# Optimization experiments

Measured on AMD Instinct MI355X. Metric: run time of the kernel, lower is better.

## Reference

```python
import jax, jax.numpy as jnp
import numpy as np


def setup_inputs() -> dict:
    key = jax.random.key(0)
    ks = jax.random.split(key, 13)
    B, CTX, H, ENC, BALL, T = 65536, 128, 64, 64, 2, 64
    IN = 2 + BALL + ENC  # 68
    s = lambda *sh: 1.0 / np.sqrt(sh[-1])
    return {
        "context": jax.random.normal(ks[0], (B, CTX), jnp.float32),
        "target_encoding": jax.random.normal(ks[1], (B, ENC), jnp.float32),
        "ball_land_xy": jax.random.normal(ks[2], (B, BALL), jnp.float32),
        "Wh_ctx": jax.random.normal(ks[3], (H, CTX), jnp.float32) * s(CTX),
        "bh_ctx": jax.random.normal(ks[4], (H,), jnp.float32) * 0.01,
        "Wc_ctx": jax.random.normal(ks[5], (H, CTX), jnp.float32) * s(CTX),
        "bc_ctx": jax.random.normal(ks[6], (H,), jnp.float32) * 0.01,
        "W_ih": jax.random.normal(ks[7], (4 * H, IN), jnp.float32) * s(IN),
        "W_hh": jax.random.normal(ks[8], (4 * H, H), jnp.float32) * s(H),
        "b_ih": jax.random.normal(ks[9], (4 * H,), jnp.float32) * 0.01,
        "b_hh": jax.random.normal(ks[10], (4 * H,), jnp.float32) * 0.01,
        "W_out": jax.random.normal(ks[11], (2, H), jnp.float32) * s(H),
        "b_out": jax.random.normal(ks[12], (2,), jnp.float32) * 0.01,
        "max_frames": T,
    }


def reference(context, target_encoding, ball_land_xy,
              Wh_ctx, bh_ctx, Wc_ctx, bc_ctx,
              W_ih, W_hh, b_ih, b_hh, W_out, b_out, max_frames):
    H = W_hh.shape[1]
    # initial hidden / cell state from fused context (num_layers=1, so squeeze the layer dim)
    h0 = context @ Wh_ctx.T + bh_ctx  # (B, H)
    c0 = context @ Wc_ctx.T + bc_ctx  # (B, H)
    B = context.shape[0]

    # decoder input per step = [prev_disp(2), ball_land_xy(2), target_encoding(64)];
    # ball/encoding part is constant across steps -> precompute its gate contribution
    W_prev = W_ih[:, :2]            # (4H, 2) columns acting on prev_disp
    W_stat = W_ih[:, 2:]            # (4H, 2+ENC)
    static = jnp.concatenate([ball_land_xy, target_encoding], axis=-1)
    gates_static = static @ W_stat.T + b_ih + b_hh  # (B, 4H)

    prev0 = jnp.zeros((B, 2), context.dtype)

    def step(carry, _):
        h, c, prev = carry
        gates = prev @ W_prev.T + h @ W_hh.T + gates_static  # (B, 4H)
        i, f, g, o = jnp.split(gates, 4, axis=-1)            # torch gate order i,f,g,o
        i = jax.nn.sigmoid(i)
        f = jax.nn.sigmoid(f)
        g = jnp.tanh(g)
        o = jax.nn.sigmoid(o)
        c = f * c + i * g
        h = o * jnp.tanh(c)
        pred = h @ W_out.T + b_out                           # (B, 2)
        # prev_disp = pred.detach() in the original
        return (h, c, jax.lax.stop_gradient(pred)), pred

    _, preds = jax.lax.scan(step, (h0, c0, prev0), None, length=max_frames)
    return jnp.transpose(preds, (1, 0, 2))  # (B, max_frames, 2)
```

## Files before the change

kernel.cpp:

```cpp
#include <hip/hip_runtime.h>
#include <hip/hip_bf16.h>
#include <stdint.h>


typedef unsigned short u16;
typedef unsigned int u32;
typedef __bf16 bf16x8 __attribute__((ext_vector_type(8)));
typedef u16 u16x8 __attribute__((ext_vector_type(8)));
typedef float f32x4 __attribute__((ext_vector_type(4)));
typedef float f32x2 __attribute__((ext_vector_type(2)));

#define MFMA16(a, b, c) __builtin_amdgcn_mfma_f32_16x16x32_bf16((a), (b), (c), 0, 0, 0)

#define SCL_SIG (-1.442695040888963f)
#define SCL_TANH (2.885390081777927f)

__device__ __forceinline__ u16 f2bf(float f) {
  __bf16 h = (__bf16)f;
  return __builtin_bit_cast(u16, h);
}
__device__ __forceinline__ float bf2f(u16 u) {
  return __builtin_bit_cast(float, ((u32)u) << 16);
}
__device__ __forceinline__ u32 pkbf(float lo, float hi) {
  union { __bf16 b[2]; u32 u; } p;
  p.b[0] = (__bf16)lo;
  p.b[1] = (__bf16)hi;
  return p.u;
}
__device__ __forceinline__ bf16x8 ldfrag_g(const u16* p) {
  u16x8 v = *(const u16x8*)p;
  return __builtin_bit_cast(bf16x8, v);
}
__device__ __forceinline__ void split8(const float* v, bf16x8& hi, bf16x8& lo) {
  union { u16 s[8]; bf16x8 b; } H, L;
#pragma unroll
  for (int i = 0; i < 8; i++) {
    u16 h = f2bf(v[i]);
    H.s[i] = h;
    L.s[i] = f2bf(v[i] - bf2f(h));
  }
  hi = H.b;
  lo = L.b;
}

__device__ __forceinline__ void nonlin4(const f32x4 ai, const f32x4 af, const f32x4 ag,
                                        const f32x4 ao, f32x4& crow, u32& w0h, u32& w1h,
                                        u32& w0l, u32& w1l) {
  float hi[4], lo[4];
#pragma unroll
  for (int q = 0; q < 4; q++) {
    float iv = __builtin_amdgcn_rcpf(1.f + __builtin_amdgcn_exp2f(ai[q]));
    float fv = __builtin_amdgcn_rcpf(1.f + __builtin_amdgcn_exp2f(af[q]));
    float ov = __builtin_amdgcn_rcpf(1.f + __builtin_amdgcn_exp2f(ao[q]));
    float rg = __builtin_amdgcn_rcpf(1.f + __builtin_amdgcn_exp2f(ag[q]));
    float gv = __builtin_fmaf(rg, -2.f, 1.f);
    float cc = __builtin_fmaf(fv, crow[q], iv * gv);
    crow[q] = cc;
    float r2 = __builtin_amdgcn_rcpf(1.f + __builtin_amdgcn_exp2f(cc * SCL_TANH));
    float hh = __builtin_fmaf(r2, ov * -2.f, ov);
    u16 h16 = f2bf(hh);
    hi[q] = bf2f(h16);
    lo[q] = hh - hi[q];
  }
  w0h = pkbf(hi[0], hi[1]);
  w1h = pkbf(hi[2], hi[3]);
  w0l = pkbf(lo[0], lo[1]);
  w1l = pkbf(lo[2], lo[3]);
}

__global__ void setup_k(const float* __restrict__ Wh_ctx, const float* __restrict__ Wc_ctx,
                        const float* __restrict__ W_ih, const float* __restrict__ W_hh,
                        const float* __restrict__ b_ih, const float* __restrict__ b_hh,
                        const float* __restrict__ W_out, const float* __restrict__ b_out,
                        u16* __restrict__ weffH, u16* __restrict__ weffL,
                        u16* __restrict__ whhH, u16* __restrict__ whhL,
                        u16* __restrict__ wstatH, u16* __restrict__ wstatL,
                        u16* __restrict__ whcH, u16* __restrict__ whcL,
                        u16* __restrict__ wccH, u16* __restrict__ wccL,
                        float* __restrict__ bsum, float* __restrict__ wpbv) {
  int gr = (int)threadIdx.x;
  const int gate = gr >> 6;
  const float s = (gate == 2) ? SCL_TANH : SCL_SIG;
  float wp0 = W_ih[gr * 68 + 0];
  float wp1 = W_ih[gr * 68 + 1];
  for (int k = 0; k < 64; k++) {
    float whh = s * W_hh[gr * 64 + k];
    u16 h = f2bf(whh);
    whhH[gr * 64 + k] = h;
    whhL[gr * 64 + k] = f2bf(whh - bf2f(h));
    float we = s * (W_hh[gr * 64 + k] + wp0 * W_out[k] + wp1 * W_out[64 + k]);
    u16 eh = f2bf(we);
    weffH[gr * 64 + k] = eh;
    weffL[gr * 64 + k] = f2bf(we - bf2f(eh));
  }
  for (int k = 0; k < 96; k++) {
    float v = (k < 66) ? s * W_ih[gr * 68 + 2 + k] : 0.f;
    u16 h = f2bf(v);
    wstatH[gr * 96 + k] = h;
    wstatL[gr * 96 + k] = f2bf(v - bf2f(h));
  }
  float wpb_ = s * (wp0 * b_out[0] + wp1 * b_out[1]);
  wpbv[gr] = wpb_;
  bsum[gr] = s * (b_ih[gr] + b_hh[gr]) + wpb_;
  if (gr < 64) {
    for (int k = 0; k < 128; k++) {
      float a = Wh_ctx[gr * 128 + k];
      u16 ah = f2bf(a);
      whcH[gr * 128 + k] = ah;
      whcL[gr * 128 + k] = f2bf(a - bf2f(ah));
      float b = Wc_ctx[gr * 128 + k];
      u16 bh_ = f2bf(b);
      wccH[gr * 128 + k] = bh_;
      wccL[gr * 128 + k] = f2bf(b - bf2f(bh_));
    }
  }
}

#define HFRAG(base, f) \
  ldfrag_g((const u16*)((const char*)(base) + c * 128 + (((16 * g) + 64 * (f)) ^ sw4)))

#define HWRITE(base, grp, w0, w1)                                \
  do {                                                           \
    char* bp_ = (char*)(base) + c * 128;                         \
    *(u32*)(bp_ + ((32 * (grp) + 8 * g) ^ sw4)) = (w0);          \
    *(u32*)(bp_ + ((32 * (grp) + 8 * g + 4) ^ sw4)) = (w1);      \
  } while (0)

__global__ __launch_bounds__(256, 3) void traj_main(
    const float* __restrict__ ctx, const float* __restrict__ enc,
    const float* __restrict__ ball, const float* __restrict__ bh,
    const float* __restrict__ bc, const float* __restrict__ bout,
    const float* __restrict__ woutf, const u16* __restrict__ weffH,
    const u16* __restrict__ weffL, const u16* __restrict__ whhH,
    const u16* __restrict__ whhL, const u16* __restrict__ wstatH,
    const u16* __restrict__ wstatL, const u16* __restrict__ whcH,
    const u16* __restrict__ whcL, const u16* __restrict__ wccH,
    const u16* __restrict__ wccL, const float* __restrict__ bsum,
    const float* __restrict__ wpbv, float* __restrict__ out) {
  __shared__ __align__(16) u16 hH_sh[2][16 * 64];
  __shared__ __align__(16) u16 hL_sh[2][16 * 64];
  __shared__ __align__(16) float p_sh[16 * 64 * 2];

  const int tid = (int)threadIdx.x;
  const int lane = tid & 63;
  const int w = tid >> 6;
  const int c = lane & 15;
  const int g = lane >> 4;
  const int sw4 = (c & 7) << 4;
  const int b0 = (int)blockIdx.x * 16;
  const size_t row = (size_t)(b0 + c);

  bf16x8 xcH[4], xcL[4];
#pragma unroll
  for (int kk = 0; kk < 4; kk++) {
    const float* p = ctx + row * 128 + 32 * kk + 8 * g;
    f32x4 a = *(const f32x4*)p;
    f32x4 b = *(const f32x4*)(p + 4);
    float v[8] = {a[0], a[1], a[2], a[3], b[0], b[1], b[2], b[3]};
    split8(v, xcH[kk], xcL[kk]);
  }

  {
    f32x4 acc = *(const f32x4*)(bh + 16 * w + 4 * g);
#pragma unroll
    for (int kk = 0; kk < 4; kk++) {
      bf16x8 aH = ldfrag_g(whcH + (16 * w + c) * 128 + 32 * kk + 8 * g);
      bf16x8 aL = ldfrag_g(whcL + (16 * w + c) * 128 + 32 * kk + 8 * g);
      acc = MFMA16(aH, xcH[kk], acc);
      acc = MFMA16(aH, xcL[kk], acc);
      acc = MFMA16(aL, xcH[kk], acc);
    }
    float hi_[4], lo_[4];
#pragma unroll
    for (int q = 0; q < 4; q++) {
      u16 h16 = f2bf(acc[q]);
      hi_[q] = bf2f(h16);
      lo_[q] = acc[q] - hi_[q];
    }
    HWRITE(hH_sh[0], w, pkbf(hi_[0], hi_[1]), pkbf(hi_[2], hi_[3]));
    HWRITE(hL_sh[0], w, pkbf(lo_[0], lo_[1]), pkbf(lo_[2], lo_[3]));
  }

  f32x4 cst;
  {
    f32x4 acc = *(const f32x4*)(bc + 16 * w + 4 * g);
#pragma unroll
    for (int kk = 0; kk < 4; kk++) {
      bf16x8 aH = ldfrag_g(wccH + (16 * w + c) * 128 + 32 * kk + 8 * g);
      bf16x8 aL = ldfrag_g(wccL + (16 * w + c) * 128 + 32 * kk + 8 * g);
      acc = MFMA16(aH, xcH[kk], acc);
      acc = MFMA16(aH, xcL[kk], acc);
      acc = MFMA16(aL, xcH[kk], acc);
    }
    cst = acc;
  }

  bf16x8 xsH[3], xsL[3];
#pragma unroll
  for (int kk = 0; kk < 3; kk++) {
    float v[8];
#pragma unroll
    for (int j = 0; j < 8; j++) {
      int k = 32 * kk + 8 * g + j;
      float val = 0.f;
      if (k < 2) val = ball[row * 2 + k];
      else if (k < 66) val = enc[row * 64 + (k - 2)];
      v[j] = val;
    }
    split8(v, xsH[kk], xsL[kk]);
  }

  f32x4 gsf[4];
#pragma unroll
  for (int j = 0; j < 4; j++) {
    const int tl = 4 * j + w;
    f32x4 acc = *(const f32x4*)(bsum + 16 * tl + 4 * g);
#pragma unroll
    for (int kk = 0; kk < 3; kk++) {
      bf16x8 aH = ldfrag_g(wstatH + (16 * tl + c) * 96 + 32 * kk + 8 * g);
      bf16x8 aL = ldfrag_g(wstatL + (16 * tl + c) * 96 + 32 * kk + 8 * g);
      acc = MFMA16(aH, xsH[kk], acc);
      acc = MFMA16(aH, xsL[kk], acc);
      acc = MFMA16(aL, xsH[kk], acc);
    }
    gsf[j] = acc;
  }

  bf16x8 wof[2];
#pragma unroll
  for (int f = 0; f < 2; f++) {
    float v[8];
#pragma unroll
    for (int j = 0; j < 8; j++) {
      int k = 32 * f + 8 * g + j;
      v[j] = (c < 2) ? woutf[c * 64 + k] : 0.f;
    }
    bf16x8 dummy;
    split8(v, wof[f], dummy);
  }
  const float bo0 = bout[0], bo1 = bout[1];

  bf16x8 wfH[4][2], wfL[4][2];
#pragma unroll
  for (int j = 0; j < 4; j++) {
    const int tl = 4 * j + w;
#pragma unroll
    for (int f = 0; f < 2; f++) {
      wfH[j][f] = ldfrag_g(weffH + (16 * tl + c) * 64 + 32 * f + 8 * g);
      wfL[j][f] = ldfrag_g(weffL + (16 * tl + c) * 64 + 32 * f + 8 * g);
    }
  }

  __syncthreads();

  {
    bf16x8 hh0 = HFRAG(hH_sh[0], 0), hh1 = HFRAG(hH_sh[0], 1);
    bf16x8 hl0 = HFRAG(hL_sh[0], 0), hl1 = HFRAG(hL_sh[0], 1);
    f32x4 av[4];
#pragma unroll
    for (int j = 0; j < 4; j++) {
      const int tl = 4 * j + w;
      f32x4 acc = gsf[j] - *(const f32x4*)(wpbv + 16 * tl + 4 * g);
      bf16x8 aH0 = ldfrag_g(whhH + (16 * tl + c) * 64 + 8 * g);
      bf16x8 aH1 = ldfrag_g(whhH + (16 * tl + c) * 64 + 32 + 8 * g);
      bf16x8 aL0 = ldfrag_g(whhL + (16 * tl + c) * 64 + 8 * g);
      bf16x8 aL1 = ldfrag_g(whhL + (16 * tl + c) * 64 + 32 + 8 * g);
      acc = MFMA16(aH0, hh0, acc);
      acc = MFMA16(aH1, hh1, acc);
      acc = MFMA16(aH0, hl0, acc);
      acc = MFMA16(aH1, hl1, acc);
      acc = MFMA16(aL0, hh0, acc);
      acc = MFMA16(aL1, hh1, acc);
      av[j] = acc;
    }
    u32 w0h, w1h, w0l, w1l;
    nonlin4(av[0], av[1], av[2], av[3], cst, w0h, w1h, w0l, w1l);
    HWRITE(hH_sh[1], w, w0h, w1h);
    HWRITE(hL_sh[1], w, w0l, w1l);
    __syncthreads();
  }

#pragma unroll 1
  for (int k = 1; k < 64; k++) {
    const int rb = k & 1, wb = rb ^ 1;
    bf16x8 hh0 = HFRAG(hH_sh[rb], 0), hh1 = HFRAG(hH_sh[rb], 1);
    bf16x8 hl0 = HFRAG(hL_sh[rb], 0), hl1 = HFRAG(hL_sh[rb], 1);
    if (((k - 1) & 3) == w) {
      f32x4 pacc = {bo0, bo1, 0.f, 0.f};
      pacc = MFMA16(wof[0], hh0, pacc);
      pacc = MFMA16(wof[1], hh1, pacc);
      if (g == 0) {
        f32x2 pr = {pacc[0], pacc[1]};
        *(f32x2*)((char*)p_sh + c * 512 + (((k - 1) * 8) ^ ((c & 7) << 3))) = pr;
      }
    }
    f32x4 av[4];
#pragma unroll
    for (int j = 0; j < 4; j++) {
      f32x4 acc = gsf[j];
      acc = MFMA16(wfH[j][0], hh0, acc);
      acc = MFMA16(wfH[j][1], hh1, acc);
      acc = MFMA16(wfH[j][0], hl0, acc);
      acc = MFMA16(wfH[j][1], hl1, acc);
      acc = MFMA16(wfL[j][0], hh0, acc);
      acc = MFMA16(wfL[j][1], hh1, acc);
      av[j] = acc;
    }
    u32 w0h, w1h, w0l, w1l;
    nonlin4(av[0], av[1], av[2], av[3], cst, w0h, w1h, w0l, w1l);
    HWRITE(hH_sh[wb], w, w0h, w1h);
    HWRITE(hL_sh[wb], w, w0l, w1l);
    __syncthreads();
  }

  if (w == 3) {
    bf16x8 hh0 = HFRAG(hH_sh[0], 0), hh1 = HFRAG(hH_sh[0], 1);
    f32x4 pacc = {bo0, bo1, 0.f, 0.f};
    pacc = MFMA16(wof[0], hh0, pacc);
    pacc = MFMA16(wof[1], hh1, pacc);
    if (g == 0) {
      f32x2 pr = {pacc[0], pacc[1]};
      *(f32x2*)((char*)p_sh + c * 512 + ((63 * 8) ^ ((c & 7) << 3))) = pr;
    }
  }
  __syncthreads();

#pragma unroll
  for (int p = 0; p < 4; p++) {
    const int r = 4 * p + w;
    f32x2 v = *(const f32x2*)((const char*)p_sh + r * 512 + ((lane * 8) ^ ((r & 7) << 3)));
    *(f32x2*)(out + (size_t)(b0 + r) * 128 + lane * 2) = v;
  }
}

extern "C" void kernel_launch(void* const* d_in, const int* in_sizes, int n_in,
                              void* d_out, int out_size, void* d_ws, size_t ws_size,
                              hipStream_t stream) {
  const float* ctx = (const float*)d_in[0];
  const float* enc = (const float*)d_in[1];
  const float* ball = (const float*)d_in[2];
  const float* Wh = (const float*)d_in[3];
  const float* bh = (const float*)d_in[4];
  const float* Wc = (const float*)d_in[5];
  const float* bc = (const float*)d_in[6];
  const float* Wih = (const float*)d_in[7];
  const float* Whh = (const float*)d_in[8];
  const float* bih = (const float*)d_in[9];
  const float* bhh = (const float*)d_in[10];
  const float* Wout = (const float*)d_in[11];
  const float* bout = (const float*)d_in[12];
  float* out = (float*)d_out;

  char* ws = (char*)d_ws;
  u16* weffH = (u16*)(ws + 0);
  u16* weffL = (u16*)(ws + 32768);
  u16* whhH = (u16*)(ws + 65536);
  u16* whhL = (u16*)(ws + 98304);
  u16* wstatH = (u16*)(ws + 131072);
  u16* wstatL = (u16*)(ws + 180224);
  u16* whcH = (u16*)(ws + 229376);
  u16* whcL = (u16*)(ws + 245760);
  u16* wccH = (u16*)(ws + 262144);
  u16* wccL = (u16*)(ws + 278528);
  float* bsum = (float*)(ws + 294912);
  float* wpbv = (float*)(ws + 295936);

  const int B = in_sizes[0] / 128;

  setup_k<<<1, 256, 0, stream>>>(Wh, Wc, Wih, Whh, bih, bhh, Wout, bout, weffH, weffL,
                                 whhH, whhL, wstatH, wstatL, whcH, whcL, wccH, wccL,
                                 bsum, wpbv);
  traj_main<<<B / 16, 256, 0, stream>>>(ctx, enc, ball, bh, bc, bout, Wout, weffH, weffL,
                                        whhH, whhL, wstatH, wstatL, whcH, whcL, wccH,
                                        wccL, bsum, wpbv, out);
}
```

Before: 633.9 us.

## Process two independent 16-row batch tiles per block to interleave recurrent chains

Each block now handles 32 batch rows as two independent 16-row tiles (A and B) that share the register-resident weight fragments and barriers. Interleaving two independent MFMA dependency chains per step is meant to hide MFMA and nonlinearity latency, and it halves the number of barriers per unit of work. In exchange register pressure roughly doubles, so launch bounds drop from 3 to 2 blocks per CU and the grid halves, which lowers occupancy.

```diff
diff --git a/kernel.cpp b/kernel.cpp
--- a/kernel.cpp
+++ b/kernel.cpp
@@ -127,7 +127,7 @@
     *(u32*)(bp_ + ((32 * (grp) + 8 * g + 4) ^ sw4)) = (w1);      \
   } while (0)
 
-__global__ __launch_bounds__(256, 3) void traj_main(
+__global__ __launch_bounds__(256, 2) void traj_main(
     const float* __restrict__ ctx, const float* __restrict__ enc,
     const float* __restrict__ ball, const float* __restrict__ bh,
     const float* __restrict__ bc, const float* __restrict__ bout,
@@ -138,9 +138,9 @@
     const u16* __restrict__ whcL, const u16* __restrict__ wccH,
     const u16* __restrict__ wccL, const float* __restrict__ bsum,
     const float* __restrict__ wpbv, float* __restrict__ out) {
-  __shared__ __align__(16) u16 hH_sh[2][16 * 64];
-  __shared__ __align__(16) u16 hL_sh[2][16 * 64];
-  __shared__ __align__(16) float p_sh[16 * 64 * 2];
+  __shared__ __align__(16) u16 hH_sh[2][2][16 * 64];
+  __shared__ __align__(16) u16 hL_sh[2][2][16 * 64];
+  __shared__ __align__(16) float p_sh[2][16 * 64 * 2];
 
   const int tid = (int)threadIdx.x;
   const int lane = tid & 63;
@@ -148,83 +148,119 @@
   const int c = lane & 15;
   const int g = lane >> 4;
   const int sw4 = (c & 7) << 4;
-  const int b0 = (int)blockIdx.x * 16;
-  const size_t row = (size_t)(b0 + c);
-
-  bf16x8 xcH[4], xcL[4];
+  const int b0 = (int)blockIdx.x * 32;
+  const size_t rowA = (size_t)(b0 + c);
+  const size_t rowB = (size_t)(b0 + 16 + c);
+
+  bf16x8 xcHA[4], xcLA[4], xcHB[4], xcLB[4];
 #pragma unroll
   for (int kk = 0; kk < 4; kk++) {
-    const float* p = ctx + row * 128 + 32 * kk + 8 * g;
-    f32x4 a = *(const f32x4*)p;
-    f32x4 b = *(const f32x4*)(p + 4);
-    float v[8] = {a[0], a[1], a[2], a[3], b[0], b[1], b[2], b[3]};
-    split8(v, xcH[kk], xcL[kk]);
+    {
+      const float* p = ctx + rowA * 128 + 32 * kk + 8 * g;
+      f32x4 a = *(const f32x4*)p;
+      f32x4 b = *(const f32x4*)(p + 4);
+      float v[8] = {a[0], a[1], a[2], a[3], b[0], b[1], b[2], b[3]};
+      split8(v, xcHA[kk], xcLA[kk]);
+    }
+    {
+      const float* p = ctx + rowB * 128 + 32 * kk + 8 * g;
+      f32x4 a = *(const f32x4*)p;
+      f32x4 b = *(const f32x4*)(p + 4);
+      float v[8] = {a[0], a[1], a[2], a[3], b[0], b[1], b[2], b[3]};
+      split8(v, xcHB[kk], xcLB[kk]);
+    }
   }
 
   {
-    f32x4 acc = *(const f32x4*)(bh + 16 * w + 4 * g);
+    f32x4 accA = *(const f32x4*)(bh + 16 * w + 4 * g);
+    f32x4 accB = accA;
 #pragma unroll
     for (int kk = 0; kk < 4; kk++) {
       bf16x8 aH = ldfrag_g(whcH + (16 * w + c) * 128 + 32 * kk + 8 * g);
       bf16x8 aL = ldfrag_g(whcL + (16 * w + c) * 128 + 32 * kk + 8 * g);
-      acc = MFMA16(aH, xcH[kk], acc);
-      acc = MFMA16(aH, xcL[kk], acc);
-      acc = MFMA16(aL, xcH[kk], acc);
-    }
-    float hi_[4], lo_[4];
+      accA = MFMA16(aH, xcHA[kk], accA);
+      accA = MFMA16(aH, xcLA[kk], accA);
+      accA = MFMA16(aL, xcHA[kk], accA);
+      accB = MFMA16(aH, xcHB[kk], accB);
+      accB = MFMA16(aH, xcLB[kk], accB);
+      accB = MFMA16(aL, xcHB[kk], accB);
+    }
+    float hiA[4], loA[4], hiB[4], loB[4];
 #pragma unroll
     for (int q = 0; q < 4; q++) {
-      u16 h16 = f2bf(acc[q]);
-      hi_[q] = bf2f(h16);
-      lo_[q] = acc[q] - hi_[q];
-    }
-    HWRITE(hH_sh[0], w, pkbf(hi_[0], hi_[1]), pkbf(hi_[2], hi_[3]));
-    HWRITE(hL_sh[0], w, pkbf(lo_[0], lo_[1]), pkbf(lo_[2], lo_[3]));
-  }
-
-  f32x4 cst;
+      u16 hA = f2bf(accA[q]);
+      hiA[q] = bf2f(hA);
+      loA[q] = accA[q] - hiA[q];
+      u16 hB = f2bf(accB[q]);
+      hiB[q] = bf2f(hB);
+      loB[q] = accB[q] - hiB[q];
+    }
+    HWRITE(hH_sh[0][0], w, pkbf(hiA[0], hiA[1]), pkbf(hiA[2], hiA[3]));
+    HWRITE(hL_sh[0][0], w, pkbf(loA[0], loA[1]), pkbf(loA[2], loA[3]));
+    HWRITE(hH_sh[1][0], w, pkbf(hiB[0], hiB[1]), pkbf(hiB[2], hiB[3]));
+    HWRITE(hL_sh[1][0], w, pkbf(loB[0], loB[1]), pkbf(loB[2], loB[3]));
+  }
+
+  f32x4 cstA, cstB;
   {
-    f32x4 acc = *(const f32x4*)(bc + 16 * w + 4 * g);
+    f32x4 accA = *(const f32x4*)(bc + 16 * w + 4 * g);
+    f32x4 accB = accA;
 #pragma unroll
     for (int kk = 0; kk < 4; kk++) {
       bf16x8 aH = ldfrag_g(wccH + (16 * w + c) * 128 + 32 * kk + 8 * g);
       bf16x8 aL = ldfrag_g(wccL + (16 * w + c) * 128 + 32 * kk + 8 * g);
-      acc = MFMA16(aH, xcH[kk], acc);
-      acc = MFMA16(aH, xcL[kk], acc);
-      acc = MFMA16(aL, xcH[kk], acc);
-    }
-    cst = acc;
-  }
-
-  bf16x8 xsH[3], xsL[3];
+      accA = MFMA16(aH, xcHA[kk], accA);
+      accA = MFMA16(aH, xcLA[kk], accA);
+      accA = MFMA16(aL, xcHA[kk], accA);
+      accB = MFMA16(aH, xcHB[kk], accB);
+      accB = MFMA16(aH, xcLB[kk], accB);
+      accB = MFMA16(aL, xcHB[kk], accB);
+    }
+    cstA = accA;
+    cstB = accB;
+  }
+
+  bf16x8 xsHA[3], xsLA[3], xsHB[3], xsLB[3];
 #pragma unroll
   for (int kk = 0; kk < 3; kk++) {
-    float v[8];
+    float vA[8], vB[8];
 #pragma unroll
     for (int j = 0; j < 8; j++) {
       int k = 32 * kk + 8 * g + j;
-      float val = 0.f;
-      if (k < 2) val = ball[row * 2 + k];
-      else if (k < 66) val = enc[row * 64 + (k - 2)];
-      v[j] = val;
-    }
-    split8(v, xsH[kk], xsL[kk]);
-  }
-
-  f32x4 gsf[4];
+      float a = 0.f, b = 0.f;
+      if (k < 2) {
+        a = ball[rowA * 2 + k];
+        b = ball[rowB * 2 + k];
+      } else if (k < 66) {
+        a = enc[rowA * 64 + (k - 2)];
+        b = enc[rowB * 64 + (k - 2)];
+      }
+      vA[j] = a;
+      vB[j] = b;
+    }
+    split8(vA, xsHA[kk], xsLA[kk]);
+    split8(vB, xsHB[kk], xsLB[kk]);
+  }
+
+  f32x4 gsfA[4], gsfB[4];
 #pragma unroll
   for (int j = 0; j < 4; j++) {
     const int tl = 4 * j + w;
-    f32x4 acc = *(const f32x4*)(bsum + 16 * tl + 4 * g);
+    f32x4 accA = *(const f32x4*)(bsum + 16 * tl + 4 * g);
+    f32x4 accB = accA;
 #pragma unroll
     for (int kk = 0; kk < 3; kk++) {
       bf16x8 aH = ldfrag_g(wstatH + (16 * tl + c) * 96 + 32 * kk + 8 * g);
       bf16x8 aL = ldfrag_g(wstatL + (16 * tl + c) * 96 + 32 * kk + 8 * g);
-      acc = MFMA16(aH, xsH[kk], acc);
-      acc = MFMA16(aH, xsL[kk], acc);
-      acc = MFMA16(aL, xsH[kk], acc);
-    }
-    gsf[j] = acc;
+      accA = MFMA16(aH, xsHA[kk], accA);
+      accA = MFMA16(aH, xsLA[kk], accA);
+      accA = MFMA16(aL, xsHA[kk], accA);
+      accB = MFMA16(aH, xsHB[kk], accB);
+      accB = MFMA16(aH, xsLB[kk], accB);
+      accB = MFMA16(aL, xsHB[kk], accB);
+    }
+    gsfA[j] = accA;
+    gsfB[j] = accB;
   }
 
   bf16x8 wof[2];
@@ -255,82 +291,127 @@
   __syncthreads();
 
   {
-    bf16x8 hh0 = HFRAG(hH_sh[0], 0), hh1 = HFRAG(hH_sh[0], 1);
-    bf16x8 hl0 = HFRAG(hL_sh[0], 0), hl1 = HFRAG(hL_sh[0], 1);
-    f32x4 av[4];
+    bf16x8 hhA0 = HFRAG(hH_sh[0][0], 0), hhA1 = HFRAG(hH_sh[0][0], 1);
+    bf16x8 hlA0 = HFRAG(hL_sh[0][0], 0), hlA1 = HFRAG(hL_sh[0][0], 1);
+    bf16x8 hhB0 = HFRAG(hH_sh[1][0], 0), hhB1 = HFRAG(hH_sh[1][0], 1);
+    bf16x8 hlB0 = HFRAG(hL_sh[1][0], 0), hlB1 = HFRAG(hL_sh[1][0], 1);
+    f32x4 avA[4], avB[4];
 #pragma unroll
     for (int j = 0; j < 4; j++) {
       const int tl = 4 * j + w;
-      f32x4 acc = gsf[j] - *(const f32x4*)(wpbv + 16 * tl + 4 * g);
+      f32x4 base = *(const f32x4*)(wpbv + 16 * tl + 4 * g);
+      f32x4 accA = gsfA[j] - base;
+      f32x4 accB = gsfB[j] - base;
       bf16x8 aH0 = ldfrag_g(whhH + (16 * tl + c) * 64 + 8 * g);
       bf16x8 aH1 = ldfrag_g(whhH + (16 * tl + c) * 64 + 32 + 8 * g);
       bf16x8 aL0 = ldfrag_g(whhL + (16 * tl + c) * 64 + 8 * g);
       bf16x8 aL1 = ldfrag_g(whhL + (16 * tl + c) * 64 + 32 + 8 * g);
-      acc = MFMA16(aH0, hh0, acc);
-      acc = MFMA16(aH1, hh1, acc);
-      acc = MFMA16(aH0, hl0, acc);
-      acc = MFMA16(aH1, hl1, acc);
-      acc = MFMA16(aL0, hh0, acc);
-      acc = MFMA16(aL1, hh1, acc);
-      av[j] = acc;
+      accA = MFMA16(aH0, hhA0, accA);
+      accA = MFMA16(aH1, hhA1, accA);
+      accA = MFMA16(aH0, hlA0, accA);
+      accA = MFMA16(aH1, hlA1, accA);
+      accA = MFMA16(aL0, hhA0, accA);
+      accA = MFMA16(aL1, hhA1, accA);
+      accB = MFMA16(aH0, hhB0, accB);
+      accB = MFMA16(aH1, hhB1, accB);
+      accB = MFMA16(aH0, hlB0, accB);
+      accB = MFMA16(aH1, hlB1, accB);
+      accB = MFMA16(aL0, hhB0, accB);
+      accB = MFMA16(aL1, hhB1, accB);
+      avA[j] = accA;
+      avB[j] = accB;
     }
     u32 w0h, w1h, w0l, w1l;
-    nonlin4(av[0], av[1], av[2], av[3], cst, w0h, w1h, w0l, w1l);
-    HWRITE(hH_sh[1], w, w0h, w1h);
-    HWRITE(hL_sh[1], w, w0l, w1l);
+    nonlin4(avA[0], avA[1], avA[2], avA[3], cstA, w0h, w1h, w0l, w1l);
+    HWRITE(hH_sh[0][1], w, w0h, w1h);
+    HWRITE(hL_sh[0][1], w, w0l, w1l);
+    nonlin4(avB[0], avB[1], avB[2], avB[3], cstB, w0h, w1h, w0l, w1l);
+    HWRITE(hH_sh[1][1], w, w0h, w1h);
+    HWRITE(hL_sh[1][1], w, w0l, w1l);
     __syncthreads();
   }
 
 #pragma unroll 1
   for (int k = 1; k < 64; k++) {
     const int rb = k & 1, wb = rb ^ 1;
-    bf16x8 hh0 = HFRAG(hH_sh[rb], 0), hh1 = HFRAG(hH_sh[rb], 1);
-    bf16x8 hl0 = HFRAG(hL_sh[rb], 0), hl1 = HFRAG(hL_sh[rb], 1);
+    bf16x8 hhA0 = HFRAG(hH_sh[0][rb], 0), hhA1 = HFRAG(hH_sh[0][rb], 1);
+    bf16x8 hlA0 = HFRAG(hL_sh[0][rb], 0), hlA1 = HFRAG(hL_sh[0][rb], 1);
+    bf16x8 hhB0 = HFRAG(hH_sh[1][rb], 0), hhB1 = HFRAG(hH_sh[1][rb], 1);
+    bf16x8 hlB0 = HFRAG(hL_sh[1][rb], 0), hlB1 = HFRAG(hL_sh[1][rb], 1);
     if (((k - 1) & 3) == w) {
-      f32x4 pacc = {bo0, bo1, 0.f, 0.f};
-      pacc = MFMA16(wof[0], hh0, pacc);
-      pacc = MFMA16(wof[1], hh1, pacc);
+      f32x4 pA = {bo0, bo1, 0.f, 0.f};
+      pA = MFMA16(wof[0], hhA0, pA);
+      pA = MFMA16(wof[1], hhA1, pA);
+      f32x4 pB = {bo0, bo1, 0.f, 0.f};
+      pB = MFMA16(wof[0], hhB0, pB);
+      pB = MFMA16(wof[1], hhB1, pB);
       if (g == 0) {
-        f32x2 pr = {pacc[0], pacc[1]};
-        *(f32x2*)((char*)p_sh + c * 512 + (((k - 1) * 8) ^ ((c & 7) << 3))) = pr;
+        f32x2 prA = {pA[0], pA[1]};
+        *(f32x2*)((char*)&p_sh[0][0] + c * 512 + (((k - 1) * 8) ^ ((c & 7) << 3))) = prA;
+        f32x2 prB = {pB[0], pB[1]};
+        *(f32x2*)((char*)&p_sh[1][0] + c * 512 + (((k - 1) * 8) ^ ((c & 7) << 3))) = prB;
       }
     }
-    f32x4 av[4];
+    f32x4 avA[4], avB[4];
 #pragma unroll
     for (int j = 0; j < 4; j++) {
-      f32x4 acc = gsf[j];
-      acc = MFMA16(wfH[j][0], hh0, acc);
-      acc = MFMA16(wfH[j][1], hh1, acc);
-      acc = MFMA16(wfH[j][0], hl0, acc);
-      acc = MFMA16(wfH[j][1], hl1, acc);
-      acc = MFMA16(wfL[j][0], hh0, acc);
-      acc = MFMA16(wfL[j][1], hh1, acc);
-      av[j] = acc;
+      f32x4 acc = gsfA[j];
+      acc = MFMA16(wfH[j][0], hhA0, acc);
+      acc = MFMA16(wfH[j][1], hhA1, acc);
+      acc = MFMA16(wfH[j][0], hlA0, acc);
+      acc = MFMA16(wfH[j][1], hlA1, acc);
+      acc = MFMA16(wfL[j][0], hhA0, acc);
+      acc = MFMA16(wfL[j][1], hhA1, acc);
+      avA[j] = acc;
+    }
+#pragma unroll
+    for (int j = 0; j < 4; j++) {
+      f32x4 acc = gsfB[j];
+      acc = MFMA16(wfH[j][0], hhB0, acc);
+      acc = MFMA16(wfH[j][1], hhB1, acc);
+      acc = MFMA16(wfH[j][0], hlB0, acc);
+      acc = MFMA16(wfH[j][1], hlB1, acc);
+      acc = MFMA16(wfL[j][0], hhB0, acc);
+      acc = MFMA16(wfL[j][1], hhB1, acc);
+      avB[j] = acc;
     }
     u32 w0h, w1h, w0l, w1l;
-    nonlin4(av[0], av[1], av[2], av[3], cst, w0h, w1h, w0l, w1l);
-    HWRITE(hH_sh[wb], w, w0h, w1h);
-    HWRITE(hL_sh[wb], w, w0l, w1l);
+    nonlin4(avA[0], avA[1], avA[2], avA[3], cstA, w0h, w1h, w0l, w1l);
+    HWRITE(hH_sh[0][wb], w, w0h, w1h);
+    HWRITE(hL_sh[0][wb], w, w0l, w1l);
+    nonlin4(avB[0], avB[1], avB[2], avB[3], cstB, w0h, w1h, w0l, w1l);
+    HWRITE(hH_sh[1][wb], w, w0h, w1h);
+    HWRITE(hL_sh[1][wb], w, w0l, w1l);
     __syncthreads();
   }
 
   if (w == 3) {
-    bf16x8 hh0 = HFRAG(hH_sh[0], 0), hh1 = HFRAG(hH_sh[0], 1);
-    f32x4 pacc = {bo0, bo1, 0.f, 0.f};
-    pacc = MFMA16(wof[0], hh0, pacc);
-    pacc = MFMA16(wof[1], hh1, pacc);
+    bf16x8 hhA0 = HFRAG(hH_sh[0][0], 0), hhA1 = HFRAG(hH_sh[0][0], 1);
+    bf16x8 hhB0 = HFRAG(hH_sh[1][0], 0), hhB1 = HFRAG(hH_sh[1][0], 1);
+    f32x4 pA = {bo0, bo1, 0.f, 0.f};
+    pA = MFMA16(wof[0], hhA0, pA);
+    pA = MFMA16(wof[1], hhA1, pA);
+    f32x4 pB = {bo0, bo1, 0.f, 0.f};
+    pB = MFMA16(wof[0], hhB0, pB);
+    pB = MFMA16(wof[1], hhB1, pB);
     if (g == 0) {
-      f32x2 pr = {pacc[0], pacc[1]};
-      *(f32x2*)((char*)p_sh + c * 512 + ((63 * 8) ^ ((c & 7) << 3))) = pr;
+      f32x2 prA = {pA[0], pA[1]};
+      *(f32x2*)((char*)&p_sh[0][0] + c * 512 + ((63 * 8) ^ ((c & 7) << 3))) = prA;
+      f32x2 prB = {pB[0], pB[1]};
+      *(f32x2*)((char*)&p_sh[1][0] + c * 512 + ((63 * 8) ^ ((c & 7) << 3))) = prB;
     }
   }
   __syncthreads();
 
 #pragma unroll
-  for (int p = 0; p < 4; p++) {
-    const int r = 4 * p + w;
-    f32x2 v = *(const f32x2*)((const char*)p_sh + r * 512 + ((lane * 8) ^ ((r & 7) << 3)));
-    *(f32x2*)(out + (size_t)(b0 + r) * 128 + lane * 2) = v;
+  for (int t = 0; t < 2; t++) {
+#pragma unroll
+    for (int p = 0; p < 4; p++) {
+      const int r = 4 * p + w;
+      f32x2 v =
+          *(const f32x2*)((const char*)&p_sh[t][0] + r * 512 + ((lane * 8) ^ ((r & 7) << 3)));
+      *(f32x2*)(out + (size_t)(b0 + 16 * t + r) * 128 + lane * 2) = v;
+    }
   }
 }
 
@@ -371,7 +452,7 @@
   setup_k<<<1, 256, 0, stream>>>(Wh, Wc, Wih, Whh, bih, bhh, Wout, bout, weffH, weffL,
                                  whhH, whhL, wstatH, wstatL, whcH, whcL, wccH, wccL,
                                  bsum, wpbv);
-  traj_main<<<B / 16, 256, 0, stream>>>(ctx, enc, ball, bh, bc, bout, Wout, weffH, weffL,
+  traj_main<<<B / 32, 256, 0, stream>>>(ctx, enc, ball, bh, bc, bout, Wout, weffH, weffL,
                                         whhH, whhL, wstatH, wstatL, whcH, whcL, wccH,
                                         wccL, bsum, wpbv, out);
 }
```

Result: no change. 639.3 us (+0.9%).
